# Performance work log

Hardware: AMD Instinct MI355X
Metric: run time of the kernel (lower is better)

The kernel has to match this reference:

```python
import jax, jax.numpy as jnp
import numpy as np

B, N, DK, DV = 16, 4096, 64, 64


def setup_inputs() -> dict:
    key = jax.random.key(0)
    kq, kk, kv = jax.random.split(key, 3)
    q = jax.random.normal(kq, (B, N, DK), dtype=jnp.float32)
    k = jax.random.normal(kk, (B, N, DK), dtype=jnp.float32)
    v = jax.random.normal(kv, (B, N, DV), dtype=jnp.float32)
    # causal mask: positions j<=i are attendable (mask==True)
    mask = jnp.tril(jnp.ones((N, N), dtype=bool))[None, :, :]  # (1, N, N)
    return {"q": q, "k": k, "v": v, "mask": mask}


def reference(q, k, v, mask):
    # scores: (B, N, N)
    scale = 1.0 / jnp.sqrt(jnp.asarray(q.shape[-1], dtype=q.dtype))
    scores = jnp.einsum('bnd,bmd->bnm', q, k) * scale
    scores = jnp.where(mask, scores, jnp.asarray(-jnp.inf, dtype=scores.dtype))
    attn = jax.nn.softmax(scores, axis=-1)
    # dropout is identity in eval/reference mode
    return jnp.einsum('bnm,bmd->bnd', attn, v)
```

## Files before the change

### kernel.cpp

```cpp
#include <hip/hip_runtime.h>


#define N_SEQ 4096
#define DIM   64

typedef __bf16  bf16x8 __attribute__((ext_vector_type(8)));
typedef unsigned short u16x8 __attribute__((ext_vector_type(8)));
typedef float   f32x4  __attribute__((ext_vector_type(4)));
typedef short   short4v __attribute__((ext_vector_type(4)));

__device__ int g_qcount[8];

static __device__ __forceinline__ unsigned short f2bf(float f) {
    unsigned int u = __float_as_uint(f);
    u += 0x7FFFu + ((u >> 16) & 1u);
    return (unsigned short)(u >> 16);
}

static __device__ __forceinline__ unsigned int pk2bf(float a, float b) {
#if defined(__HIP_DEVICE_COMPILE__) && __has_builtin(__builtin_amdgcn_cvt_pk_bf16_f32)
    typedef __bf16 bf16x2_t __attribute__((ext_vector_type(2)));
    bf16x2_t r = __builtin_amdgcn_cvt_pk_bf16_f32(a, b);
    return __builtin_bit_cast(unsigned int, r);
#else
    return (unsigned int)f2bf(a) | ((unsigned int)f2bf(b) << 16);
#endif
}

static __device__ __forceinline__ float fexp2(float x) {
#if defined(__HIP_DEVICE_COMPILE__) && __has_builtin(__builtin_amdgcn_exp2f)
    return __builtin_amdgcn_exp2f(x);
#else
    return exp2f(x);
#endif
}

static __device__ __forceinline__ bf16x8 ld_frag(const void* p) {
    u16x8 u = *reinterpret_cast<const u16x8*>(p);
    return __builtin_bit_cast(bf16x8, u);
}

static __device__ __forceinline__ f32x4 mfma_pv(uint2 a, uint2 b, f32x4 c) {
#if defined(__HIP_DEVICE_COMPILE__)
#if __has_builtin(__builtin_amdgcn_mfma_f32_16x16x16bf16_1k)
    return __builtin_amdgcn_mfma_f32_16x16x16bf16_1k(
        __builtin_bit_cast(short4v, a), __builtin_bit_cast(short4v, b), c, 0, 0, 0);
#else
    f32x4 d;
    asm volatile("v_mfma_f32_16x16x16_bf16 %0, %1, %2, %3"
                 : "=v"(d) : "v"(a), "v"(b), "v"(c));
    return d;
#endif
#else
    (void)a; (void)b;
    return c;
#endif
}

static __device__ __forceinline__ void gl_lds16(const unsigned short* g, unsigned short* l) {
#if defined(__HIP_DEVICE_COMPILE__)
    __builtin_amdgcn_global_load_lds(
        (const __attribute__((address_space(1))) unsigned int*)(g),
        (__attribute__((address_space(3))) unsigned int*)(l), 16, 0, 0);
#else
    (void)g; (void)l;
#endif
}

__global__ __launch_bounds__(256)
void prep_kv(const float* __restrict__ K, const float* __restrict__ V,
             unsigned short* __restrict__ wsK, unsigned short* __restrict__ wsV) {
    if (blockIdx.x == 0 && blockIdx.y == 0 && blockIdx.z == 0 && threadIdx.x < 8)
        g_qcount[threadIdx.x] = 0;
    const int b = blockIdx.y, t = blockIdx.x;
    if (blockIdx.z == 0) {
        const float* src = K + ((size_t)b * N_SEQ + t * 64) * DIM;
        unsigned short* dst = wsK + ((size_t)(b * 64 + t)) * 4096;
        #pragma unroll
        for (int ph = 0; ph < 2; ++ph) {
            const int gidx = threadIdx.x + ph * 256;
            const int r = gidx >> 3, g = gidx & 7;
            const float* p = src + r * DIM + g * 8;
            f32x4 f0 = *reinterpret_cast<const f32x4*>(p);
            f32x4 f1 = *reinterpret_cast<const f32x4*>(p + 4);
            uint4 w;
            w.x = pk2bf(f0[0], f0[1]); w.y = pk2bf(f0[2], f0[3]);
            w.z = pk2bf(f1[0], f1[1]); w.w = pk2bf(f1[2], f1[3]);
            *reinterpret_cast<uint4*>(&dst[(r * 8 + (g ^ (r & 7))) * 8]) = w;
        }
    } else {
        const int dv = threadIdx.x & 63;
        const int g0 = threadIdx.x >> 6;
        const float* src = V + ((size_t)b * N_SEQ + t * 64) * DIM + dv;
        unsigned short* dst = wsV + ((size_t)(b * 64 + t)) * 4096;
        #pragma unroll
        for (int ph = 0; ph < 2; ++ph) {
            const int g = g0 + ph * 4;
            float p[8];
            #pragma unroll
            for (int i = 0; i < 8; ++i)
                p[i] = src[(size_t)(g * 8 + i) * DIM];
            uint4 w;
            w.x = pk2bf(p[0], p[1]); w.y = pk2bf(p[2], p[3]);
            w.z = pk2bf(p[4], p[5]); w.w = pk2bf(p[6], p[7]);
            *reinterpret_cast<uint4*>(&dst[(dv * 8 + (g ^ (dv & 7))) * 8]) = w;
        }
    }
}

__global__ __launch_bounds__(256)
void attn_fwd(const float* __restrict__ Q, const unsigned short* __restrict__ wsK,
              const unsigned short* __restrict__ wsV, float* __restrict__ O) {
    __shared__ unsigned short kbuf[2][4096];
    __shared__ unsigned short vbuf[2][4096];
    __shared__ int s_item;

    const int tid  = threadIdx.x;
    const int wave = tid >> 6;
    const int lane = tid & 63;
    const int quad = lane >> 4;
    const int ln   = lane & 15;
    const int ln7  = lane & 7;
    const int r    = (int)blockIdx.x & 7;

    int kaddr[8];
    #pragma unroll
    for (int s = 0; s < 2; ++s)
        #pragma unroll
        for (int nt = 0; nt < 4; ++nt)
            kaddr[s * 4 + nt] = (nt * 16 + ln) * 128 + (((s * 4 + quad) ^ ln7) * 16);
    int vaddr[16];
    #pragma unroll
    for (int nt = 0; nt < 4; ++nt)
        #pragma unroll
        for (int dvt = 0; dvt < 4; ++dvt)
            vaddr[nt * 4 + dvt] = (dvt * 16 + ln) * 128
                                + (((nt * 2 + (quad >> 1)) ^ ln7) * 16) + (quad & 1) * 8;

    const int dma_off = wave * 1024 + lane * 8;
    const uint2 ones  = make_uint2(0x3F803F80u, 0x3F803F80u);
    const float QS = 0.125f * 1.44269504f;

    for (;;) {
        __syncthreads();
        if (tid == 0) s_item = atomicAdd(&g_qcount[r], 1);
        __syncthreads();
        const int item = s_item;
        if (item >= 128) break;

        const int tile = 63 - (item >> 1);
        const int b    = r * 2 + (item & 1);
        const int i0   = tile * 64;
        const int tmax = tile;

        const float* qptr = Q + ((size_t)b * N_SEQ + i0 + wave * 16 + ln) * DIM;
        u16x8 qa[2];
        #pragma unroll
        for (int s = 0; s < 2; ++s) {
            const float* p = qptr + s * 32 + quad * 8;
            f32x4 f0 = *reinterpret_cast<const f32x4*>(p);
            f32x4 f1 = *reinterpret_cast<const f32x4*>(p + 4);
            #pragma unroll
            for (int jj = 0; jj < 4; ++jj) {
                qa[s][jj]     = f2bf(f0[jj] * QS);
                qa[s][4 + jj] = f2bf(f1[jj] * QS);
            }
        }

        const unsigned short* kt_src = wsK + (size_t)b * 64 * 4096;
        const unsigned short* vt_src = wsV + (size_t)b * 64 * 4096;

        auto dma = [&](int t, int bufi) {
            const unsigned short* ks = kt_src + (size_t)t * 4096 + dma_off;
            const unsigned short* vs = vt_src + (size_t)t * 4096 + dma_off;
            #pragma unroll
            for (int i = 0; i < 2; ++i) {
                gl_lds16(ks + i * 512, &kbuf[bufi][wave * 1024 + i * 512]);
                gl_lds16(vs + i * 512, &vbuf[bufi][wave * 1024 + i * 512]);
            }
        };

        f32x4 o_acc[4] = {};
        f32x4 lacc = {};

        auto compute = [&](int t, const unsigned short* kb, const unsigned short* vb) {
            f32x4 st[4] = {};
            #pragma unroll
            for (int s = 0; s < 2; ++s) {
                bf16x8 qf = __builtin_bit_cast(bf16x8, qa[s]);
                #pragma unroll
                for (int nt = 0; nt < 4; ++nt) {
                    bf16x8 kf = ld_frag((const char*)kb + kaddr[s * 4 + nt]);
                    st[nt] = __builtin_amdgcn_mfma_f32_16x16x32_bf16(kf, qf, st[nt], 0, 0, 0);
                }
            }
            uint2 bvv[16];
            #pragma unroll
            for (int i = 0; i < 16; ++i)
                bvv[i] = *reinterpret_cast<const uint2*>((const char*)vb + vaddr[i]);

            uint2 pk_d[4];
            if (t == tmax) {
                const int qloc = wave * 16 + ln;
                #pragma unroll
                for (int nt = 0; nt < 4; ++nt) {
                    float p0 = fexp2((nt * 16 + quad * 4 + 0 > qloc) ? -3.0e38f : st[nt][0]);
                    float p1 = fexp2((nt * 16 + quad * 4 + 1 > qloc) ? -3.0e38f : st[nt][1]);
                    float p2 = fexp2((nt * 16 + quad * 4 + 2 > qloc) ? -3.0e38f : st[nt][2]);
                    float p3 = fexp2((nt * 16 + quad * 4 + 3 > qloc) ? -3.0e38f : st[nt][3]);
                    pk_d[nt].x = pk2bf(p0, p1);
                    pk_d[nt].y = pk2bf(p2, p3);
                }
            } else {
                #pragma unroll
                for (int nt = 0; nt < 4; ++nt) {
                    pk_d[nt].x = pk2bf(fexp2(st[nt][0]), fexp2(st[nt][1]));
                    pk_d[nt].y = pk2bf(fexp2(st[nt][2]), fexp2(st[nt][3]));
                }
            }
            #pragma unroll
            for (int nt = 0; nt < 4; ++nt) {
                #pragma unroll
                for (int dvt = 0; dvt < 4; ++dvt)
                    o_acc[dvt] = mfma_pv(pk_d[nt], bvv[nt * 4 + dvt], o_acc[dvt]);
                lacc = mfma_pv(pk_d[nt], ones, lacc);
            }
        };

        dma(0, 0);
        int t = 0;
        while (true) {
            __syncthreads();
            if (t < tmax) dma(t + 1, 1);
            compute(t, kbuf[0], vbuf[0]);
            if (t == tmax) break;
            ++t;
            __syncthreads();
            if (t < tmax) dma(t + 1, 0);
            compute(t, kbuf[1], vbuf[1]);
            if (t == tmax) break;
            ++t;
        }

        float* obase = O + ((size_t)b * N_SEQ + i0 + wave * 16) * DIM;
        #pragma unroll
        for (int rr = 0; rr < 4; ++rr) {
            const float inv = 1.0f / lacc[rr];
            #pragma unroll
            for (int dvt = 0; dvt < 4; ++dvt)
                obase[(quad * 4 + rr) * DIM + dvt * 16 + ln] = o_acc[dvt][rr] * inv;
        }
    }
}

extern "C" void kernel_launch(void* const* d_in, const int* in_sizes, int n_in,
                              void* d_out, int out_size, void* d_ws, size_t ws_size,
                              hipStream_t stream) {
    const float* q = (const float*)d_in[0];
    const float* k = (const float*)d_in[1];
    const float* v = (const float*)d_in[2];
    float* out = (float*)d_out;

    unsigned short* wsK = (unsigned short*)d_ws;
    unsigned short* wsV = wsK + (size_t)16 * 64 * 4096;

    prep_kv<<<dim3(64, 16, 2), dim3(256), 0, stream>>>(k, v, wsK, wsV);
    attn_fwd<<<dim3(512), dim3(256), 0, stream>>>(q, wsK, wsV, out);
}
```

Measured before the change: 202.8 us.

## Process 128-key KV tiles per iteration with wider V fragment loads

Doubles the key/value tile streamed per pipeline step from 64 to 128 keys. This halves the number of barriers and loop iterations and gives more MFMA work between syncs. V is repacked in the prep kernel with a permuted key order, so one 16-byte LDS read feeds two PV MFMAs instead of separate 8-byte reads. In exchange, LDS per block doubles, which lowers occupancy. For even query tiles the final chunk also computes 64 keys that are fully masked.

```diff
diff --git a/kernel.cpp b/kernel.cpp
--- a/kernel.cpp
+++ b/kernel.cpp
@@ -95,15 +95,18 @@
         unsigned short* dst = wsV + ((size_t)(b * 64 + t)) * 4096;
         #pragma unroll
         for (int ph = 0; ph < 2; ++ph) {
-            const int g = g0 + ph * 4;
+            const int gp = g0 + ph * 4;
             float p[8];
             #pragma unroll
-            for (int i = 0; i < 8; ++i)
-                p[i] = src[(size_t)(g * 8 + i) * DIM];
+            for (int e = 0; e < 8; ++e) {
+                const int pos = gp * 8 + e;
+                const int kp  = ((pos >> 2) & 3) * 16 + (pos >> 4) * 4 + (pos & 3);
+                p[e] = src[(size_t)kp * DIM];
+            }
             uint4 w;
             w.x = pk2bf(p[0], p[1]); w.y = pk2bf(p[2], p[3]);
             w.z = pk2bf(p[4], p[5]); w.w = pk2bf(p[6], p[7]);
-            *reinterpret_cast<uint4*>(&dst[(dv * 8 + (g ^ (dv & 7))) * 8]) = w;
+            *reinterpret_cast<uint4*>(&dst[(dv * 8 + (gp ^ (dv & 7))) * 8]) = w;
         }
     }
 }
@@ -111,8 +114,8 @@
 __global__ __launch_bounds__(256)
 void attn_fwd(const float* __restrict__ Q, const unsigned short* __restrict__ wsK,
               const unsigned short* __restrict__ wsV, float* __restrict__ O) {
-    __shared__ unsigned short kbuf[2][4096];
-    __shared__ unsigned short vbuf[2][4096];
+    __shared__ unsigned short kbuf[2][8192];
+    __shared__ unsigned short vbuf[2][8192];
     __shared__ int s_item;
 
     const int tid  = threadIdx.x;
@@ -123,21 +126,24 @@
     const int ln7  = lane & 7;
     const int r    = (int)blockIdx.x & 7;
 
-    int kaddr[8];
+    int kaddr[2][8];
     #pragma unroll
     for (int s = 0; s < 2; ++s)
         #pragma unroll
-        for (int nt = 0; nt < 4; ++nt)
-            kaddr[s * 4 + nt] = (nt * 16 + ln) * 128 + (((s * 4 + quad) ^ ln7) * 16);
-    int vaddr[16];
+        for (int nt = 0; nt < 8; ++nt)
+            kaddr[s][nt] = (nt >> 2) * 8192 + ((nt & 3) * 16 + ln) * 128
+                         + (((s * 4 + quad) ^ ln7) * 16);
+    int vaddr[2][2][4];
     #pragma unroll
-    for (int nt = 0; nt < 4; ++nt)
-        #pragma unroll
-        for (int dvt = 0; dvt < 4; ++dvt)
-            vaddr[nt * 4 + dvt] = (dvt * 16 + ln) * 128
-                                + (((nt * 2 + (quad >> 1)) ^ ln7) * 16) + (quad & 1) * 8;
-
-    const int dma_off = wave * 1024 + lane * 8;
+    for (int h = 0; h < 2; ++h)
+        #pragma unroll
+        for (int c = 0; c < 2; ++c)
+            #pragma unroll
+            for (int dvt = 0; dvt < 4; ++dvt)
+                vaddr[h][c][dvt] = h * 8192 + (dvt * 16 + ln) * 128
+                                 + ((((quad << 1) | c) ^ ln7) * 16);
+
+    const int dma_off = wave * 2048 + lane * 8;
     const uint2 ones  = make_uint2(0x3F803F80u, 0x3F803F80u);
     const float QS = 0.125f * 1.44269504f;
 
@@ -151,7 +157,9 @@
         const int tile = 63 - (item >> 1);
         const int b    = r * 2 + (item & 1);
         const int i0   = tile * 64;
-        const int tmax = tile;
+        const int n2   = (tile >> 1) + 1;
+        const int t2max = n2 - 1;
+        const int qloc  = tile * 64 + wave * 16 + ln;
 
         const float* qptr = Q + ((size_t)b * N_SEQ + i0 + wave * 16 + ln) * DIM;
         u16x8 qa[2];
@@ -170,76 +178,82 @@
         const unsigned short* kt_src = wsK + (size_t)b * 64 * 4096;
         const unsigned short* vt_src = wsV + (size_t)b * 64 * 4096;
 
-        auto dma = [&](int t, int bufi) {
-            const unsigned short* ks = kt_src + (size_t)t * 4096 + dma_off;
-            const unsigned short* vs = vt_src + (size_t)t * 4096 + dma_off;
-            #pragma unroll
-            for (int i = 0; i < 2; ++i) {
-                gl_lds16(ks + i * 512, &kbuf[bufi][wave * 1024 + i * 512]);
-                gl_lds16(vs + i * 512, &vbuf[bufi][wave * 1024 + i * 512]);
+        auto dma = [&](int t2, int bufi) {
+            const unsigned short* ks = kt_src + (size_t)t2 * 8192 + dma_off;
+            const unsigned short* vs = vt_src + (size_t)t2 * 8192 + dma_off;
+            #pragma unroll
+            for (int i = 0; i < 4; ++i) {
+                gl_lds16(ks + i * 512, &kbuf[bufi][wave * 2048 + i * 512]);
+                gl_lds16(vs + i * 512, &vbuf[bufi][wave * 2048 + i * 512]);
             }
         };
 
         f32x4 o_acc[4] = {};
         f32x4 lacc = {};
 
-        auto compute = [&](int t, const unsigned short* kb, const unsigned short* vb) {
-            f32x4 st[4] = {};
+        auto compute = [&](int t2, const unsigned short* kb, const unsigned short* vb) {
+            f32x4 st[8] = {};
             #pragma unroll
             for (int s = 0; s < 2; ++s) {
                 bf16x8 qf = __builtin_bit_cast(bf16x8, qa[s]);
                 #pragma unroll
-                for (int nt = 0; nt < 4; ++nt) {
-                    bf16x8 kf = ld_frag((const char*)kb + kaddr[s * 4 + nt]);
+                for (int nt = 0; nt < 8; ++nt) {
+                    bf16x8 kf = ld_frag((const char*)kb + kaddr[s][nt]);
                     st[nt] = __builtin_amdgcn_mfma_f32_16x16x32_bf16(kf, qf, st[nt], 0, 0, 0);
                 }
             }
-            uint2 bvv[16];
-            #pragma unroll
-            for (int i = 0; i < 16; ++i)
-                bvv[i] = *reinterpret_cast<const uint2*>((const char*)vb + vaddr[i]);
-
-            uint2 pk_d[4];
-            if (t == tmax) {
-                const int qloc = wave * 16 + ln;
-                #pragma unroll
-                for (int nt = 0; nt < 4; ++nt) {
-                    float p0 = fexp2((nt * 16 + quad * 4 + 0 > qloc) ? -3.0e38f : st[nt][0]);
-                    float p1 = fexp2((nt * 16 + quad * 4 + 1 > qloc) ? -3.0e38f : st[nt][1]);
-                    float p2 = fexp2((nt * 16 + quad * 4 + 2 > qloc) ? -3.0e38f : st[nt][2]);
-                    float p3 = fexp2((nt * 16 + quad * 4 + 3 > qloc) ? -3.0e38f : st[nt][3]);
+            uint2 pk_d[8];
+            if (t2 == t2max) {
+                const int kbase = t2 * 128 + quad * 4;
+                #pragma unroll
+                for (int nt = 0; nt < 8; ++nt) {
+                    const int kp = kbase + (nt >> 2) * 64 + (nt & 3) * 16;
+                    float p0 = fexp2((kp + 0 > qloc) ? -3.0e38f : st[nt][0]);
+                    float p1 = fexp2((kp + 1 > qloc) ? -3.0e38f : st[nt][1]);
+                    float p2 = fexp2((kp + 2 > qloc) ? -3.0e38f : st[nt][2]);
+                    float p3 = fexp2((kp + 3 > qloc) ? -3.0e38f : st[nt][3]);
                     pk_d[nt].x = pk2bf(p0, p1);
                     pk_d[nt].y = pk2bf(p2, p3);
                 }
             } else {
                 #pragma unroll
-                for (int nt = 0; nt < 4; ++nt) {
+                for (int nt = 0; nt < 8; ++nt) {
                     pk_d[nt].x = pk2bf(fexp2(st[nt][0]), fexp2(st[nt][1]));
                     pk_d[nt].y = pk2bf(fexp2(st[nt][2]), fexp2(st[nt][3]));
                 }
             }
             #pragma unroll
-            for (int nt = 0; nt < 4; ++nt) {
-                #pragma unroll
-                for (int dvt = 0; dvt < 4; ++dvt)
-                    o_acc[dvt] = mfma_pv(pk_d[nt], bvv[nt * 4 + dvt], o_acc[dvt]);
+            for (int h = 0; h < 2; ++h)
+                #pragma unroll
+                for (int c = 0; c < 2; ++c) {
+                    #pragma unroll
+                    for (int dvt = 0; dvt < 4; ++dvt) {
+                        uint4 bv = *reinterpret_cast<const uint4*>(
+                            (const char*)vb + vaddr[h][c][dvt]);
+                        o_acc[dvt] = mfma_pv(pk_d[h * 4 + 2 * c],
+                                             make_uint2(bv.x, bv.y), o_acc[dvt]);
+                        o_acc[dvt] = mfma_pv(pk_d[h * 4 + 2 * c + 1],
+                                             make_uint2(bv.z, bv.w), o_acc[dvt]);
+                    }
+                }
+            #pragma unroll
+            for (int nt = 0; nt < 8; ++nt)
                 lacc = mfma_pv(pk_d[nt], ones, lacc);
-            }
         };
 
         dma(0, 0);
-        int t = 0;
+        int t2 = 0;
         while (true) {
             __syncthreads();
-            if (t < tmax) dma(t + 1, 1);
-            compute(t, kbuf[0], vbuf[0]);
-            if (t == tmax) break;
-            ++t;
+            if (t2 < t2max) dma(t2 + 1, 1);
+            compute(t2, kbuf[0], vbuf[0]);
+            if (t2 == t2max) break;
+            ++t2;
             __syncthreads();
-            if (t < tmax) dma(t + 1, 0);
-            compute(t, kbuf[1], vbuf[1]);
-            if (t == tmax) break;
-            ++t;
+            if (t2 < t2max) dma(t2 + 1, 0);
+            compute(t2, kbuf[1], vbuf[1]);
+            if (t2 == t2max) break;
+            ++t2;
         }
 
         float* obase = O + ((size_t)b * N_SEQ + i0 + wave * 16) * DIM;
```

Result: faster. 198.1 us (-2.3%).

## Split long causal query tiles across two workgroups and merge in a reduce kernel

Applied to the files above, without the earlier changes.

The upper 32 query tiles of each batch are now split into two halves along the key dimension. Each half runs as a separate work item that writes unnormalized partial outputs and row sums to workspace, and a new norm_out kernel adds the two halves and normalizes them. The grid is doubled, and V is pre-permuted so each PV step can use one 16-byte LDS read per two MFMAs instead of separate 8-byte reads. The aim is better load balance and shorter critical paths, at the cost of extra workspace traffic and a third kernel launch. Skipping the running max is still valid here because the scores are bounded.

```diff
diff --git a/kernel.cpp b/kernel.cpp
--- a/kernel.cpp
+++ b/kernel.cpp
@@ -95,22 +95,26 @@
         unsigned short* dst = wsV + ((size_t)(b * 64 + t)) * 4096;
         #pragma unroll
         for (int ph = 0; ph < 2; ++ph) {
-            const int g = g0 + ph * 4;
+            const int gp = g0 + ph * 4;
             float p[8];
             #pragma unroll
-            for (int i = 0; i < 8; ++i)
-                p[i] = src[(size_t)(g * 8 + i) * DIM];
+            for (int e = 0; e < 8; ++e) {
+                const int pos = gp * 8 + e;
+                const int kp  = ((pos >> 2) & 3) * 16 + (pos >> 4) * 4 + (pos & 3);
+                p[e] = src[(size_t)kp * DIM];
+            }
             uint4 w;
             w.x = pk2bf(p[0], p[1]); w.y = pk2bf(p[2], p[3]);
             w.z = pk2bf(p[4], p[5]); w.w = pk2bf(p[6], p[7]);
-            *reinterpret_cast<uint4*>(&dst[(dv * 8 + (g ^ (dv & 7))) * 8]) = w;
+            *reinterpret_cast<uint4*>(&dst[(dv * 8 + (gp ^ (dv & 7))) * 8]) = w;
         }
     }
 }
 
 __global__ __launch_bounds__(256)
 void attn_fwd(const float* __restrict__ Q, const unsigned short* __restrict__ wsK,
-              const unsigned short* __restrict__ wsV, float* __restrict__ O) {
+              const unsigned short* __restrict__ wsV, float* __restrict__ O,
+              float* __restrict__ wsO, float* __restrict__ wsL) {
     __shared__ unsigned short kbuf[2][4096];
     __shared__ unsigned short vbuf[2][4096];
     __shared__ int s_item;
@@ -123,19 +127,18 @@
     const int ln7  = lane & 7;
     const int r    = (int)blockIdx.x & 7;
 
-    int kaddr[8];
+    int kaddr[2][4];
     #pragma unroll
     for (int s = 0; s < 2; ++s)
         #pragma unroll
         for (int nt = 0; nt < 4; ++nt)
-            kaddr[s * 4 + nt] = (nt * 16 + ln) * 128 + (((s * 4 + quad) ^ ln7) * 16);
-    int vaddr[16];
+            kaddr[s][nt] = (nt * 16 + ln) * 128 + (((s * 4 + quad) ^ ln7) * 16);
+    int vaddr[2][4];
     #pragma unroll
-    for (int nt = 0; nt < 4; ++nt)
+    for (int c = 0; c < 2; ++c)
         #pragma unroll
         for (int dvt = 0; dvt < 4; ++dvt)
-            vaddr[nt * 4 + dvt] = (dvt * 16 + ln) * 128
-                                + (((nt * 2 + (quad >> 1)) ^ ln7) * 16) + (quad & 1) * 8;
+            vaddr[c][dvt] = (dvt * 16 + ln) * 128 + ((((quad << 1) | c) ^ ln7) * 16);
 
     const int dma_off = wave * 1024 + lane * 8;
     const uint2 ones  = make_uint2(0x3F803F80u, 0x3F803F80u);
@@ -146,12 +149,30 @@
         if (tid == 0) s_item = atomicAdd(&g_qcount[r], 1);
         __syncthreads();
         const int item = s_item;
-        if (item >= 128) break;
-
-        const int tile = 63 - (item >> 1);
-        const int b    = r * 2 + (item & 1);
-        const int i0   = tile * 64;
-        const int tmax = tile;
+        if (item >= 192) break;
+
+        int tt, b, kt0, kt1, half;
+        bool partial;
+        if (item < 128) {
+            tt   = 63 - (item >> 2);
+            b    = r * 2 + ((item >> 1) & 1);
+            half = item & 1;
+            const int d  = tt + 1;
+            const int h0 = (d + 1) >> 1;
+            kt0 = half ? h0 : 0;
+            kt1 = half ? d  : h0;
+            partial = true;
+        } else {
+            const int i2 = item - 128;
+            tt   = 31 - (i2 >> 1);
+            b    = r * 2 + (i2 & 1);
+            half = 0;
+            kt0  = 0;
+            kt1  = tt + 1;
+            partial = false;
+        }
+        const int i0   = tt * 64;
+        const int qloc = i0 + wave * 16 + ln;
 
         const float* qptr = Q + ((size_t)b * N_SEQ + i0 + wave * 16 + ln) * DIM;
         u16x8 qa[2];
@@ -170,9 +191,9 @@
         const unsigned short* kt_src = wsK + (size_t)b * 64 * 4096;
         const unsigned short* vt_src = wsV + (size_t)b * 64 * 4096;
 
-        auto dma = [&](int t, int bufi) {
-            const unsigned short* ks = kt_src + (size_t)t * 4096 + dma_off;
-            const unsigned short* vs = vt_src + (size_t)t * 4096 + dma_off;
+        auto dma = [&](int kt, int bufi) {
+            const unsigned short* ks = kt_src + (size_t)kt * 4096 + dma_off;
+            const unsigned short* vs = vt_src + (size_t)kt * 4096 + dma_off;
             #pragma unroll
             for (int i = 0; i < 2; ++i) {
                 gl_lds16(ks + i * 512, &kbuf[bufi][wave * 1024 + i * 512]);
@@ -183,31 +204,27 @@
         f32x4 o_acc[4] = {};
         f32x4 lacc = {};
 
-        auto compute = [&](int t, const unsigned short* kb, const unsigned short* vb) {
+        auto compute = [&](int kt, const unsigned short* kb, const unsigned short* vb) {
             f32x4 st[4] = {};
             #pragma unroll
             for (int s = 0; s < 2; ++s) {
                 bf16x8 qf = __builtin_bit_cast(bf16x8, qa[s]);
                 #pragma unroll
                 for (int nt = 0; nt < 4; ++nt) {
-                    bf16x8 kf = ld_frag((const char*)kb + kaddr[s * 4 + nt]);
+                    bf16x8 kf = ld_frag((const char*)kb + kaddr[s][nt]);
                     st[nt] = __builtin_amdgcn_mfma_f32_16x16x32_bf16(kf, qf, st[nt], 0, 0, 0);
                 }
             }
-            uint2 bvv[16];
-            #pragma unroll
-            for (int i = 0; i < 16; ++i)
-                bvv[i] = *reinterpret_cast<const uint2*>((const char*)vb + vaddr[i]);
-
             uint2 pk_d[4];
-            if (t == tmax) {
-                const int qloc = wave * 16 + ln;
+            if (kt == tt) {
+                const int kbase = kt * 64 + quad * 4;
                 #pragma unroll
                 for (int nt = 0; nt < 4; ++nt) {
-                    float p0 = fexp2((nt * 16 + quad * 4 + 0 > qloc) ? -3.0e38f : st[nt][0]);
-                    float p1 = fexp2((nt * 16 + quad * 4 + 1 > qloc) ? -3.0e38f : st[nt][1]);
-                    float p2 = fexp2((nt * 16 + quad * 4 + 2 > qloc) ? -3.0e38f : st[nt][2]);
-                    float p3 = fexp2((nt * 16 + quad * 4 + 3 > qloc) ? -3.0e38f : st[nt][3]);
+                    const int kp = kbase + nt * 16;
+                    float p0 = fexp2((kp + 0 > qloc) ? -3.0e38f : st[nt][0]);
+                    float p1 = fexp2((kp + 1 > qloc) ? -3.0e38f : st[nt][1]);
+                    float p2 = fexp2((kp + 2 > qloc) ? -3.0e38f : st[nt][2]);
+                    float p3 = fexp2((kp + 3 > qloc) ? -3.0e38f : st[nt][3]);
                     pk_d[nt].x = pk2bf(p0, p1);
                     pk_d[nt].y = pk2bf(p2, p3);
                 }
@@ -219,37 +236,72 @@
                 }
             }
             #pragma unroll
-            for (int nt = 0; nt < 4; ++nt) {
-                #pragma unroll
-                for (int dvt = 0; dvt < 4; ++dvt)
-                    o_acc[dvt] = mfma_pv(pk_d[nt], bvv[nt * 4 + dvt], o_acc[dvt]);
+            for (int c = 0; c < 2; ++c)
+                #pragma unroll
+                for (int dvt = 0; dvt < 4; ++dvt) {
+                    uint4 bv = *reinterpret_cast<const uint4*>(
+                        (const char*)vb + vaddr[c][dvt]);
+                    o_acc[dvt] = mfma_pv(pk_d[2 * c],     make_uint2(bv.x, bv.y), o_acc[dvt]);
+                    o_acc[dvt] = mfma_pv(pk_d[2 * c + 1], make_uint2(bv.z, bv.w), o_acc[dvt]);
+                }
+            #pragma unroll
+            for (int nt = 0; nt < 4; ++nt)
                 lacc = mfma_pv(pk_d[nt], ones, lacc);
-            }
         };
 
-        dma(0, 0);
-        int t = 0;
+        dma(kt0, 0);
+        int kt = kt0, bufi = 0;
         while (true) {
             __syncthreads();
-            if (t < tmax) dma(t + 1, 1);
-            compute(t, kbuf[0], vbuf[0]);
-            if (t == tmax) break;
-            ++t;
-            __syncthreads();
-            if (t < tmax) dma(t + 1, 0);
-            compute(t, kbuf[1], vbuf[1]);
-            if (t == tmax) break;
-            ++t;
-        }
-
-        float* obase = O + ((size_t)b * N_SEQ + i0 + wave * 16) * DIM;
-        #pragma unroll
-        for (int rr = 0; rr < 4; ++rr) {
-            const float inv = 1.0f / lacc[rr];
-            #pragma unroll
-            for (int dvt = 0; dvt < 4; ++dvt)
-                obase[(quad * 4 + rr) * DIM + dvt * 16 + ln] = o_acc[dvt][rr] * inv;
-        }
+            if (kt + 1 < kt1) dma(kt + 1, bufi ^ 1);
+            compute(kt, kbuf[bufi], vbuf[bufi]);
+            if (++kt == kt1) break;
+            bufi ^= 1;
+        }
+
+        if (!partial) {
+            float* obase = O + ((size_t)b * N_SEQ + i0 + wave * 16) * DIM;
+            #pragma unroll
+            for (int rr = 0; rr < 4; ++rr) {
+                const float inv = 1.0f / lacc[rr];
+                #pragma unroll
+                for (int dvt = 0; dvt < 4; ++dvt)
+                    obase[(quad * 4 + rr) * DIM + dvt * 16 + ln] = o_acc[dvt][rr] * inv;
+            }
+        } else {
+            float* po = wsO + (((size_t)(b * 32 + (tt - 32)) * 2 + half) * 4096)
+                      + (wave * 16) * 64;
+            float* pl = wsL + (((size_t)(b * 32 + (tt - 32)) * 2 + half) * 64)
+                      + wave * 16;
+            #pragma unroll
+            for (int rr = 0; rr < 4; ++rr) {
+                #pragma unroll
+                for (int dvt = 0; dvt < 4; ++dvt)
+                    po[(quad * 4 + rr) * 64 + dvt * 16 + ln] = o_acc[dvt][rr];
+                if (ln == 0) pl[quad * 4 + rr] = lacc[rr];
+            }
+        }
+    }
+}
+
+__global__ __launch_bounds__(256)
+void norm_out(const float* __restrict__ wsO, const float* __restrict__ wsL,
+              float* __restrict__ O) {
+    const int t = 32 + blockIdx.x, b = blockIdx.y;
+    const int row = threadIdx.x >> 2;
+    const int c0  = (threadIdx.x & 3) * 16;
+    const size_t base = (size_t)(b * 32 + (t - 32)) * 2;
+    const float* p0 = wsO + base * 4096 + row * 64 + c0;
+    const float* p1 = p0 + 4096;
+    const float* l  = wsL + base * 64;
+    const float inv = 1.0f / (l[row] + l[64 + row]);
+    float* o = O + ((size_t)b * N_SEQ + t * 64 + row) * 64 + c0;
+    #pragma unroll
+    for (int i = 0; i < 16; i += 4) {
+        f32x4 a = *reinterpret_cast<const f32x4*>(p0 + i);
+        f32x4 c = *reinterpret_cast<const f32x4*>(p1 + i);
+        f32x4 v = (a + c) * inv;
+        *reinterpret_cast<f32x4*>(o + i) = v;
     }
 }
 
@@ -263,7 +315,10 @@
 
     unsigned short* wsK = (unsigned short*)d_ws;
     unsigned short* wsV = wsK + (size_t)16 * 64 * 4096;
+    float* wsO = (float*)(wsV + (size_t)16 * 64 * 4096);
+    float* wsL = wsO + (size_t)16 * 32 * 2 * 4096;
 
     prep_kv<<<dim3(64, 16, 2), dim3(256), 0, stream>>>(k, v, wsK, wsV);
-    attn_fwd<<<dim3(512), dim3(256), 0, stream>>>(q, wsK, wsV, out);
-}
+    attn_fwd<<<dim3(1024), dim3(256), 0, stream>>>(q, wsK, wsV, out, wsO, wsL);
+    norm_out<<<dim3(32, 16), dim3(256), 0, stream>>>(wsO, wsL, out);
+}
```

Measured after the change: 202.8 us. Within noise of the previous version (-0.0%).
